# Optimization experiments

Measured on AMD Instinct MI355X. Metric: run time of the kernel, lower is better.

## Reference

```python
import jax, jax.numpy as jnp
import numpy as np

HIDDEN = 2560
N_HEADS = 16
N_KV = 4
HEAD_DIM = 256
GQA = N_HEADS // N_KV
INNER = N_HEADS * HEAD_DIM  # 4096
B, L = 2, 2048
ROPE_THETA = 1000000.0
EPS = 1e-6


def _rope_tables(seq_len, dim, theta):
    pos = np.arange(seq_len, dtype=np.float32)
    inv_freq = 1.0 / (theta ** (np.arange(0, dim, 2, dtype=np.float32) / dim))
    ang = pos[:, None] * inv_freq[None, :]          # [L, dim/2]
    ang = np.concatenate([ang, ang], axis=-1)        # [L, dim]
    return jnp.asarray(np.cos(ang)), jnp.asarray(np.sin(ang))


def setup_inputs() -> dict:
    key = jax.random.key(0)
    ks = jax.random.split(key, 6)
    hidden_states = jax.random.normal(ks[0], (B, L, HIDDEN), dtype=jnp.float32)
    cos, sin = _rope_tables(L, HEAD_DIM, ROPE_THETA)
    s = 0.02
    Wq = jax.random.normal(ks[1], (HIDDEN, 2 * INNER), dtype=jnp.float32) * s
    Wk = jax.random.normal(ks[2], (HIDDEN, N_KV * HEAD_DIM), dtype=jnp.float32) * s
    Wv = jax.random.normal(ks[3], (HIDDEN, N_KV * HEAD_DIM), dtype=jnp.float32) * s
    Wo = jax.random.normal(ks[4], (INNER, HIDDEN), dtype=jnp.float32) * s
    q_norm_w = jnp.ones((HEAD_DIM,), dtype=jnp.float32)
    k_norm_w = jnp.ones((HEAD_DIM,), dtype=jnp.float32)
    return {"hidden_states": hidden_states, "cos": cos, "sin": sin,
            "Wq": Wq, "Wk": Wk, "Wv": Wv, "Wo": Wo,
            "q_norm_w": q_norm_w, "k_norm_w": k_norm_w}


def _rms_norm(x, w):
    var = jnp.mean(jnp.square(x), axis=-1, keepdims=True)
    return x * jax.lax.rsqrt(var + EPS) * w


def _apply_rotary(x, cos, sin):
    # x: [B, H, L, D]; cos/sin: [L, D]
    d = x.shape[-1]
    x1, x2 = x[..., : d // 2], x[..., d // 2:]
    return x * cos + jnp.concatenate([-x2, x1], axis=-1) * sin


def reference(hidden_states, cos, sin, Wq, Wk, Wv, Wo, q_norm_w, k_norm_w):
    Bv, Lv, _ = hidden_states.shape
    qg = hidden_states @ Wq                              # [B, L, 2*INNER]
    q, gate = qg[..., :INNER], qg[..., INNER:]
    k = (hidden_states @ Wk).reshape(Bv, Lv, N_KV, HEAD_DIM)
    v = (hidden_states @ Wv).reshape(Bv, Lv, N_KV, HEAD_DIM)

    q = _rms_norm(q.reshape(Bv, Lv, N_HEADS, HEAD_DIM), q_norm_w).transpose(0, 2, 1, 3)  # [B,H,L,D]
    k = _rms_norm(k, k_norm_w).transpose(0, 2, 1, 3)     # [B,KV,L,D]
    v = v.transpose(0, 2, 1, 3)                          # [B,KV,L,D]

    q = _apply_rotary(q, cos, sin)
    k = _apply_rotary(k, cos, sin)

    # repeat_interleave over head dim for GQA
    k = jnp.repeat(k, GQA, axis=1)                       # [B,H,L,D]
    v = jnp.repeat(v, GQA, axis=1)

    scale = 1.0 / jnp.sqrt(jnp.float32(HEAD_DIM))
    scores = jnp.einsum('bhqd,bhkd->bhqk', q, k) * scale  # [B,H,L,L]
    causal = jnp.tril(jnp.ones((Lv, Lv), dtype=bool))
    scores = jnp.where(causal, scores, jnp.finfo(scores.dtype).min)
    attn = jax.nn.softmax(scores, axis=-1)
    out = jnp.einsum('bhqk,bhkd->bhqd', attn, v)          # [B,H,L,D]

    out = out.transpose(0, 2, 1, 3).reshape(Bv, Lv, INNER) * jax.nn.silu(gate)
    return out @ Wo
```

## Files before the change

### kernel.cpp

```cpp
#include <hip/hip_runtime.h>
#include <cstdint>
#include <cstddef>

#define NQKV 10240

typedef __bf16 bf16;
typedef __attribute__((ext_vector_type(4))) __bf16 bvec4;
typedef __attribute__((ext_vector_type(8))) __bf16 bvec8;
typedef __attribute__((ext_vector_type(4))) float fvec4;

__device__ __forceinline__ void gll16(const bf16* g, bf16* l) {
  __builtin_amdgcn_global_load_lds(
      (const __attribute__((address_space(1))) void*)g,
      (__attribute__((address_space(3))) void*)l, 16, 0, 0);
}

__global__ __launch_bounds__(256) void cvt_f32_bf16(const float* __restrict__ x,
                                                    bf16* __restrict__ y, int n) {
  int i = (blockIdx.x * 256 + threadIdx.x) * 4;
  if (i < n) {
    float4 v = *(const float4*)(x + i);
    bvec4 o;
    o.x = (bf16)v.x; o.y = (bf16)v.y; o.z = (bf16)v.z; o.w = (bf16)v.w;
    *(bvec4*)(y + i) = o;
  }
}

__global__ __launch_bounds__(256) void wtrans(const float* __restrict__ W,
                                              bf16* __restrict__ Wt, int K, int N) {
  __shared__ float t[64][65];
  int n0 = blockIdx.x * 64, k0 = blockIdx.y * 64;
  int tx = threadIdx.x & 63, tg = threadIdx.x >> 6;
#pragma unroll
  for (int i = 0; i < 16; ++i) {
    int r = tg * 16 + i;
    t[r][tx] = W[(size_t)(k0 + r) * N + n0 + tx];
  }
  __syncthreads();
#pragma unroll
  for (int i = 0; i < 16; ++i) {
    int r = tg * 16 + i;
    Wt[(size_t)(n0 + r) * K + k0 + tx] = (bf16)t[tx][r];
  }
}

__global__ __launch_bounds__(256) void vtrans(const bf16* __restrict__ QKV,
                                              bf16* __restrict__ Vt) {
  __shared__ bf16 t[64][65];
  int l0 = blockIdx.x * 64, dd0 = blockIdx.y * 64;
  int bkv = blockIdx.z, b = bkv >> 2, kv = bkv & 3;
  int tx = threadIdx.x & 63, tg = threadIdx.x >> 6;
#pragma unroll
  for (int i = 0; i < 16; ++i) {
    int r = tg * 16 + i;
    t[r][tx] = QKV[(size_t)(b * 2048 + l0 + r) * NQKV + 9216 + kv * 256 + dd0 + tx];
  }
  __syncthreads();
#pragma unroll
  for (int i = 0; i < 16; ++i) {
    int r = tg * 16 + i;
    Vt[((size_t)bkv * 256 + dd0 + r) * 2048 + l0 + tx] = t[tx][r];
  }
}

__global__ __launch_bounds__(256) void norm_rope(const bf16* __restrict__ QKV,
    const float* __restrict__ cosT, const float* __restrict__ sinT,
    const float* __restrict__ qw, const float* __restrict__ kw,
    bf16* __restrict__ Qn, bf16* __restrict__ Kn) {
  int u = blockIdx.x * 4 + (threadIdx.x >> 6);
  int lane = threadIdx.x & 63;
  int token = u / 20, slot = u - token * 20;
  int b = token >> 11, l = token & 2047;
  int d0 = lane * 4;
  const float* w;
  int col0;
  bf16* outp;
  if (slot < 16) {
    col0 = slot * 256; w = qw;
    outp = Qn + ((size_t)((b * 16 + slot) * 2048 + l)) * 256;
  } else {
    int kv = slot - 16;
    col0 = 8192 + kv * 256; w = kw;
    outp = Kn + ((size_t)((b * 4 + kv) * 2048 + l)) * 256;
  }
  bvec4 xi = *(const bvec4*)(QKV + (size_t)token * NQKV + col0 + d0);
  float x[4];
#pragma unroll
  for (int j = 0; j < 4; ++j) x[j] = (float)xi[j];
  float ss = x[0] * x[0] + x[1] * x[1] + x[2] * x[2] + x[3] * x[3];
#pragma unroll
  for (int off = 32; off; off >>= 1) ss += __shfl_xor(ss, off);
  float rn = rsqrtf(ss * (1.0f / 256.0f) + 1e-6f);
  float xn[4];
#pragma unroll
  for (int j = 0; j < 4; ++j) xn[j] = x[j] * rn * w[d0 + j];
  bvec4 o;
#pragma unroll
  for (int j = 0; j < 4; ++j) {
    float other = __shfl_xor(xn[j], 32);
    float rot = (lane < 32) ? -other : other;
    float c = cosT[(size_t)l * 256 + d0 + j];
    float s = sinT[(size_t)l * 256 + d0 + j];
    o[j] = (bf16)(xn[j] * c + rot * s);
  }
  *(bvec4*)(outp + d0) = o;
}

template <typename OutT>
__global__ __launch_bounds__(256, 2) void gemm8(const bf16* __restrict__ A,
                                                const bf16* __restrict__ B,
                                                OutT* __restrict__ C,
                                                int N, int Kd) {
  __shared__ alignas(16) bf16 smem[36864];
  int tid = threadIdx.x, wave = tid >> 6, lane = tid & 63;
  int quad = lane >> 4, l15 = lane & 15;
  int wm = wave >> 1, wn = wave & 1;
  int bm = blockIdx.y, bn = blockIdx.x;
  const bf16* Ag = A + (size_t)bm * 128 * Kd;
  const bf16* Bg = B + (size_t)bn * 256 * Kd;

  bf16* b0 = smem;
  bf16* b1 = smem + 12288;
  bf16* b2 = smem + 24576;

  int nt = Kd >> 5;
  int srow = lane >> 2;
  int sc8 = ((lane & 3) ^ ((lane >> 3) & 3)) * 8;
  int csw = (quad ^ ((l15 >> 1) & 3)) * 8;

  const fvec4 FZ = {0.f, 0.f, 0.f, 0.f};
  fvec4 acc[4][8];
#pragma unroll
  for (int i = 0; i < 4; ++i)
#pragma unroll
    for (int j = 0; j < 8; ++j) acc[i][j] = FZ;

  auto stage = [&](bf16* dst, int ktel) {
#pragma unroll
    for (int i = 0; i < 6; ++i) {
      int s = wave * 6 + i;
      if (s < 8) {
        gll16(Ag + (size_t)(s * 16 + srow) * Kd + ktel + sc8, dst + s * 512);
      } else {
        gll16(Bg + (size_t)((s - 8) * 16 + srow) * Kd + ktel + sc8,
              dst + 4096 + (s - 8) * 512);
      }
    }
  };

  stage(b0, 0);
  stage(b1, 32);

  for (int t = 0; t < nt; ++t) {
    asm volatile("s_waitcnt vmcnt(6)" ::: "memory");
    __builtin_amdgcn_s_barrier();
    const bf16* Ab = b0;
    const bf16* Bb = b0 + 4096;
    bvec8 af[4], bv[8];
#pragma unroll
    for (int mt = 0; mt < 4; ++mt)
      af[mt] = *(const bvec8*)(Ab + (wm * 64 + mt * 16 + l15) * 32 + csw);
#pragma unroll
    for (int nt2 = 0; nt2 < 8; ++nt2)
      bv[nt2] = *(const bvec8*)(Bb + (wn * 128 + nt2 * 16 + l15) * 32 + csw);
    __builtin_amdgcn_s_setprio(1);
#pragma unroll
    for (int mt = 0; mt < 2; ++mt)
#pragma unroll
      for (int nt2 = 0; nt2 < 8; ++nt2)
        acc[mt][nt2] = __builtin_amdgcn_mfma_f32_16x16x32_bf16(af[mt], bv[nt2],
                                                               acc[mt][nt2], 0, 0, 0);
    __builtin_amdgcn_s_setprio(0);
    asm volatile("s_waitcnt lgkmcnt(0)" ::: "memory");
    __builtin_amdgcn_sched_barrier(0);
    __builtin_amdgcn_s_barrier();
    int t2 = t + 2;
    if (t2 >= nt) t2 = nt - 1;
    stage(b2, t2 * 32);
    __builtin_amdgcn_s_setprio(1);
#pragma unroll
    for (int mt = 2; mt < 4; ++mt)
#pragma unroll
      for (int nt2 = 0; nt2 < 8; ++nt2)
        acc[mt][nt2] = __builtin_amdgcn_mfma_f32_16x16x32_bf16(af[mt], bv[nt2],
                                                               acc[mt][nt2], 0, 0, 0);
    __builtin_amdgcn_s_setprio(0);
    bf16* tp = b0; b0 = b1; b1 = b2; b2 = tp;
  }

#pragma unroll
  for (int mt = 0; mt < 4; ++mt)
#pragma unroll
    for (int nt2 = 0; nt2 < 8; ++nt2)
#pragma unroll
      for (int r = 0; r < 4; ++r) {
        int row = bm * 128 + wm * 64 + mt * 16 + quad * 4 + r;
        int col = bn * 256 + wn * 128 + nt2 * 16 + l15;
        C[(size_t)row * N + col] = (OutT)acc[mt][nt2][r];
      }
}

__global__ __launch_bounds__(256, 2) void flash(const bf16* __restrict__ Q,
    const bf16* __restrict__ K, const bf16* __restrict__ Vt,
    const bf16* __restrict__ QKV, bf16* __restrict__ Og) {
  __shared__ alignas(16) bf16 smem[32768];
  bf16* Ks = smem;
  bf16* Vts = smem + 16384;

  int pairi = blockIdx.x;
  int bh = blockIdx.y, b = bh >> 4, h = bh & 15, kvh = h >> 2;
  int tid = threadIdx.x, wave = tid >> 6, lane = tid & 63;
  int quad = lane >> 4, l15 = lane & 15;

  const bf16* Qh = Q + ((size_t)(b * 16 + h) * 2048) * 256;
  const bf16* Kb = K + ((size_t)(b * 4 + kvh) * 2048) * 256;
  const bf16* Vb = Vt + ((size_t)(b * 4 + kvh) * 256) * 2048;
  const fvec4 FZ = {0.f, 0.f, 0.f, 0.f};

  for (int half = 0; half < 2; ++half) {
    int qt = half ? (31 - pairi) : pairi;
    int q0 = qt * 64;

    bvec8 qf[8];
    {
      int row = q0 + wave * 16 + l15;
#pragma unroll
      for (int kk = 0; kk < 8; ++kk) {
        bvec8 v = *(const bvec8*)(Qh + (size_t)row * 256 + kk * 32 + quad * 8);
#pragma unroll
        for (int j = 0; j < 8; ++j) v[j] = (bf16)((float)v[j] * 0.0625f);
        qf[kk] = v;
      }
    }

    fvec4 acc[16];
#pragma unroll
    for (int i = 0; i < 16; ++i) acc[i] = FZ;
    float m_run[4], l_run[4];
#pragma unroll
    for (int r = 0; r < 4; ++r) { m_run[r] = -3.0e38f; l_run[r] = 0.f; }

    for (int kt = 0; kt <= qt; ++kt) {
      int k0 = kt * 64;
      __syncthreads();
#pragma unroll
      for (int i = 0; i < 8; ++i) {
        int seg = wave * 8 + i;
        int krow = seg * 2 + (lane >> 5);
        int kc = (lane & 31) ^ (krow & 31);
        gll16(Kb + (size_t)(k0 + krow) * 256 + kc * 8, Ks + seg * 512);
        int vrow = seg * 8 + (lane >> 3);
        int vc = (lane & 7) ^ (vrow & 7);
        gll16(Vb + (size_t)vrow * 2048 + k0 + vc * 8, Vts + seg * 512);
      }
      __syncthreads();

      fvec4 s[4];
#pragma unroll
      for (int nt = 0; nt < 4; ++nt) {
        s[nt] = FZ;
        int row = nt * 16 + l15;
        int rm = row & 31;
#pragma unroll
        for (int ks = 0; ks < 8; ++ks) {
          int c = ks * 4 + quad;
          bvec8 kf = *(const bvec8*)(Ks + (size_t)row * 256 + (size_t)(c ^ rm) * 8);
          s[nt] = __builtin_amdgcn_mfma_f32_16x16x32_bf16(qf[ks], kf, s[nt], 0, 0, 0);
        }
      }
      __syncthreads();

      if (kt == qt) {
#pragma unroll
        for (int nt = 0; nt < 4; ++nt)
#pragma unroll
          for (int r = 0; r < 4; ++r)
            if (k0 + nt * 16 + l15 > q0 + wave * 16 + quad * 4 + r)
              s[nt][r] = -3.0e38f;
      }

      bf16* Pw = smem + wave * 1152;
      float alpha[4];
      {
        float rs[4];
#pragma unroll
        for (int r = 0; r < 4; ++r) {
          float m = fmaxf(fmaxf(s[0][r], s[1][r]),
                          fmaxf(s[2][r], s[3][r]));
#pragma unroll
          for (int off = 8; off; off >>= 1) m = fmaxf(m, __shfl_xor(m, off));
          float Mn = fmaxf(m_run[r], m);
          alpha[r] = __expf(m_run[r] - Mn);
          m_run[r] = Mn;
          rs[r] = 0.f;
        }
#pragma unroll
        for (int nt = 0; nt < 4; ++nt)
#pragma unroll
          for (int r = 0; r < 4; ++r) {
            float p = __expf(s[nt][r] - m_run[r]);
            rs[r] += p;
            Pw[(quad * 4 + r) * 72 + nt * 16 + l15] = (bf16)p;
          }
#pragma unroll
        for (int r = 0; r < 4; ++r) {
#pragma unroll
          for (int off = 8; off; off >>= 1) rs[r] += __shfl_xor(rs[r], off);
          l_run[r] = l_run[r] * alpha[r] + rs[r];
        }
#pragma unroll
        for (int nt = 0; nt < 16; ++nt)
#pragma unroll
          for (int r = 0; r < 4; ++r) acc[nt][r] *= alpha[r];
      }
      __syncthreads();

#pragma unroll
      for (int ks = 0; ks < 2; ++ks) {
        bvec8 pf = *(const bvec8*)(Pw + l15 * 72 + ks * 32 + quad * 8);
#pragma unroll
        for (int nt = 0; nt < 16; ++nt) {
          int row = nt * 16 + l15;
          int c = ks * 4 + quad;
          bvec8 vf = *(const bvec8*)(Vts + (size_t)row * 64 + (size_t)(c ^ (row & 7)) * 8);
          acc[nt] = __builtin_amdgcn_mfma_f32_16x16x32_bf16(pf, vf, acc[nt], 0, 0, 0);
        }
      }
    }

#pragma unroll
    for (int r = 0; r < 4; ++r) {
      int token = b * 2048 + q0 + wave * 16 + quad * 4 + r;
      float inv = 1.0f / l_run[r];
#pragma unroll
      for (int nt = 0; nt < 16; ++nt) {
        int col = h * 256 + nt * 16 + l15;
        float g = (float)QKV[(size_t)token * NQKV + 4096 + col];
        float silu = g / (1.0f + __expf(-g));
        Og[(size_t)token * 4096 + col] = (bf16)(acc[nt][r] * inv * silu);
      }
    }
  }
}

extern "C" void kernel_launch(void* const* d_in, const int* in_sizes, int n_in,
                              void* d_out, int out_size, void* d_ws, size_t ws_size,
                              hipStream_t stream) {
  const float* hs   = (const float*)d_in[0];
  const float* cosT = (const float*)d_in[1];
  const float* sinT = (const float*)d_in[2];
  const float* Wq   = (const float*)d_in[3];
  const float* Wk   = (const float*)d_in[4];
  const float* Wv   = (const float*)d_in[5];
  const float* Wo   = (const float*)d_in[6];
  const float* qw   = (const float*)d_in[7];
  const float* kw   = (const float*)d_in[8];
  float* out = (float*)d_out;

  char* p = (char*)d_ws;
  auto alloc = [&](size_t bytes) {
    char* r = p;
    p += (bytes + 255) & ~(size_t)255;
    return r;
  };
  bf16* Xb    = (bf16*)alloc((size_t)4096 * 2560 * 2);
  bf16* Wqkvt = (bf16*)alloc((size_t)10240 * 2560 * 2);
  bf16* Wot   = (bf16*)alloc((size_t)2560 * 4096 * 2);
  bf16* QKV   = (bf16*)alloc((size_t)4096 * 10240 * 2);
  bf16* Qn    = (bf16*)alloc((size_t)2 * 16 * 2048 * 256 * 2);
  bf16* Kn    = (bf16*)alloc((size_t)2 * 4 * 2048 * 256 * 2);
  bf16* Vtb   = (bf16*)alloc((size_t)2 * 4 * 256 * 2048 * 2);
  bf16* Og    = (bf16*)alloc((size_t)4096 * 4096 * 2);

  cvt_f32_bf16<<<10240, 256, 0, stream>>>(hs, Xb, 4096 * 2560);
  wtrans<<<dim3(128, 40), 256, 0, stream>>>(Wq, Wqkvt, 2560, 8192);
  wtrans<<<dim3(16, 40), 256, 0, stream>>>(Wk, Wqkvt + (size_t)8192 * 2560, 2560, 1024);
  wtrans<<<dim3(16, 40), 256, 0, stream>>>(Wv, Wqkvt + (size_t)9216 * 2560, 2560, 1024);
  wtrans<<<dim3(40, 64), 256, 0, stream>>>(Wo, Wot, 4096, 2560);

  gemm8<bf16><<<dim3(40, 32), 256, 0, stream>>>(Xb, Wqkvt, QKV, 10240, 2560);

  norm_rope<<<20480, 256, 0, stream>>>(QKV, cosT, sinT, qw, kw, Qn, Kn);
  vtrans<<<dim3(32, 4, 8), 256, 0, stream>>>(QKV, Vtb);

  flash<<<dim3(16, 32), 256, 0, stream>>>(Qn, Kn, Vtb, QKV, Og);

  gemm8<float><<<dim3(10, 32), 256, 0, stream>>>(Og, Wot, out, 2560, 4096);
}
```

Baseline: 764.4 us.

## Swizzle block order, drop flash barriers with lazy rescale, restage GEMM prefetch

The GEMM now remaps block indices across 8 groups, presumably to match XCD placement. It also issues the next tile's prefetch right after the top barrier, which removes the mid-iteration barrier and the lgkmcnt wait. The flash kernel uses a similar swizzled block mapping and moves the per-wave P buffer to its own LDS region. That lets two __syncthreads calls be removed. It also rescales the running max and accumulators only when some row's max grows by more than 8, and adds setprio around the MFMA loops. The changes aim to cut barrier stalls and rescale work. The risks are LDS hazards if the remaining synchronization is not enough, plus a small rise in LDS use.

```diff
diff --git a/kernel.cpp b/kernel.cpp
--- a/kernel.cpp
+++ b/kernel.cpp
@@ -115,7 +115,11 @@
   int tid = threadIdx.x, wave = tid >> 6, lane = tid & 63;
   int quad = lane >> 4, l15 = lane & 15;
   int wm = wave >> 1, wn = wave & 1;
-  int bm = blockIdx.y, bn = blockIdx.x;
+  int nbx = gridDim.x;
+  int lin = blockIdx.x + nbx * blockIdx.y;
+  int cpx = (nbx * gridDim.y) >> 3;
+  int swz = (lin & 7) * cpx + (lin >> 3);
+  int bn = swz % nbx, bm = swz / nbx;
   const bf16* Ag = A + (size_t)bm * 128 * Kd;
   const bf16* Bg = B + (size_t)bn * 256 * Kd;
 
@@ -154,6 +158,9 @@
   for (int t = 0; t < nt; ++t) {
     asm volatile("s_waitcnt vmcnt(6)" ::: "memory");
     __builtin_amdgcn_s_barrier();
+    int t2 = t + 2;
+    if (t2 >= nt) t2 = nt - 1;
+    stage(b2, t2 * 32);
     const bf16* Ab = b0;
     const bf16* Bb = b0 + 4096;
     bvec8 af[4], bv[8];
@@ -165,21 +172,7 @@
       bv[nt2] = *(const bvec8*)(Bb + (wn * 128 + nt2 * 16 + l15) * 32 + csw);
     __builtin_amdgcn_s_setprio(1);
 #pragma unroll
-    for (int mt = 0; mt < 2; ++mt)
-#pragma unroll
-      for (int nt2 = 0; nt2 < 8; ++nt2)
-        acc[mt][nt2] = __builtin_amdgcn_mfma_f32_16x16x32_bf16(af[mt], bv[nt2],
-                                                               acc[mt][nt2], 0, 0, 0);
-    __builtin_amdgcn_s_setprio(0);
-    asm volatile("s_waitcnt lgkmcnt(0)" ::: "memory");
-    __builtin_amdgcn_sched_barrier(0);
-    __builtin_amdgcn_s_barrier();
-    int t2 = t + 2;
-    if (t2 >= nt) t2 = nt - 1;
-    stage(b2, t2 * 32);
-    __builtin_amdgcn_s_setprio(1);
-#pragma unroll
-    for (int mt = 2; mt < 4; ++mt)
+    for (int mt = 0; mt < 4; ++mt)
 #pragma unroll
       for (int nt2 = 0; nt2 < 8; ++nt2)
         acc[mt][nt2] = __builtin_amdgcn_mfma_f32_16x16x32_bf16(af[mt], bv[nt2],
@@ -203,14 +196,17 @@
 __global__ __launch_bounds__(256, 2) void flash(const bf16* __restrict__ Q,
     const bf16* __restrict__ K, const bf16* __restrict__ Vt,
     const bf16* __restrict__ QKV, bf16* __restrict__ Og) {
-  __shared__ alignas(16) bf16 smem[32768];
+  __shared__ alignas(16) bf16 smem[37376];
   bf16* Ks = smem;
   bf16* Vts = smem + 16384;
 
-  int pairi = blockIdx.x;
-  int bh = blockIdx.y, b = bh >> 4, h = bh & 15, kvh = h >> 2;
+  int lin = blockIdx.x + 16 * blockIdx.y;
+  int swz = (lin & 7) * 64 + (lin >> 3);
+  int pairi = swz & 15;
+  int bh = swz >> 4, b = bh >> 4, h = bh & 15, kvh = h >> 2;
   int tid = threadIdx.x, wave = tid >> 6, lane = tid & 63;
   int quad = lane >> 4, l15 = lane & 15;
+  bf16* Pw = smem + 32768 + wave * 1152;
 
   const bf16* Qh = Q + ((size_t)(b * 16 + h) * 2048) * 256;
   const bf16* Kb = K + ((size_t)(b * 4 + kvh) * 2048) * 256;
@@ -261,14 +257,15 @@
         s[nt] = FZ;
         int row = nt * 16 + l15;
         int rm = row & 31;
+        __builtin_amdgcn_s_setprio(1);
 #pragma unroll
         for (int ks = 0; ks < 8; ++ks) {
           int c = ks * 4 + quad;
           bvec8 kf = *(const bvec8*)(Ks + (size_t)row * 256 + (size_t)(c ^ rm) * 8);
           s[nt] = __builtin_amdgcn_mfma_f32_16x16x32_bf16(qf[ks], kf, s[nt], 0, 0, 0);
         }
-      }
-      __syncthreads();
+        __builtin_amdgcn_s_setprio(0);
+      }
 
       if (kt == qt) {
 #pragma unroll
@@ -279,21 +276,31 @@
               s[nt][r] = -3.0e38f;
       }
 
-      bf16* Pw = smem + wave * 1152;
-      float alpha[4];
       {
-        float rs[4];
+        float pmax[4];
 #pragma unroll
         for (int r = 0; r < 4; ++r) {
           float m = fmaxf(fmaxf(s[0][r], s[1][r]),
                           fmaxf(s[2][r], s[3][r]));
 #pragma unroll
           for (int off = 8; off; off >>= 1) m = fmaxf(m, __shfl_xor(m, off));
-          float Mn = fmaxf(m_run[r], m);
-          alpha[r] = __expf(m_run[r] - Mn);
-          m_run[r] = Mn;
-          rs[r] = 0.f;
-        }
+          pmax[r] = m;
+        }
+        int need = 0;
+#pragma unroll
+        for (int r = 0; r < 4; ++r) need |= (pmax[r] > m_run[r] + 8.0f) ? 1 : 0;
+        if (__any(need)) {
+#pragma unroll
+          for (int r = 0; r < 4; ++r) {
+            float Mn = fmaxf(m_run[r], pmax[r]);
+            float alpha = __expf(m_run[r] - Mn);
+            m_run[r] = Mn;
+            l_run[r] *= alpha;
+#pragma unroll
+            for (int nt = 0; nt < 16; ++nt) acc[nt][r] *= alpha;
+          }
+        }
+        float rs[4] = {0.f, 0.f, 0.f, 0.f};
 #pragma unroll
         for (int nt = 0; nt < 4; ++nt)
 #pragma unroll
@@ -306,18 +313,14 @@
         for (int r = 0; r < 4; ++r) {
 #pragma unroll
           for (int off = 8; off; off >>= 1) rs[r] += __shfl_xor(rs[r], off);
-          l_run[r] = l_run[r] * alpha[r] + rs[r];
-        }
-#pragma unroll
-        for (int nt = 0; nt < 16; ++nt)
-#pragma unroll
-          for (int r = 0; r < 4; ++r) acc[nt][r] *= alpha[r];
-      }
-      __syncthreads();
+          l_run[r] += rs[r];
+        }
+      }
 
 #pragma unroll
       for (int ks = 0; ks < 2; ++ks) {
         bvec8 pf = *(const bvec8*)(Pw + l15 * 72 + ks * 32 + quad * 8);
+        __builtin_amdgcn_s_setprio(1);
 #pragma unroll
         for (int nt = 0; nt < 16; ++nt) {
           int row = nt * 16 + l15;
@@ -325,6 +328,7 @@
           bvec8 vf = *(const bvec8*)(Vts + (size_t)row * 64 + (size_t)(c ^ (row & 7)) * 8);
           acc[nt] = __builtin_amdgcn_mfma_f32_16x16x32_bf16(pf, vf, acc[nt], 0, 0, 0);
         }
+        __builtin_amdgcn_s_setprio(0);
       }
     }
 
```

Result: no change. 765.1 us (+0.1%).
